# Performance work log

Hardware: AMD Instinct MI355X
Metric: run time of the kernel (lower is better)

Reference implementation:

```python
import jax, jax.numpy as jnp
import numpy as np

E = 1024
H = 16
DH = E // H
FF = 4 * E
EPS = 1e-5


def _layer_norm(x, g, b):
    mu = jnp.mean(x, axis=-1, keepdims=True)
    var = jnp.var(x, axis=-1, keepdims=True)
    return (x - mu) * jax.lax.rsqrt(var + EPS) * g + b


def setup_inputs() -> dict:
    key = jax.random.key(0)
    ks = jax.random.split(key, 12)
    B, S = 2, 2048
    s_e = 1.0 / np.sqrt(E)
    s_f = 1.0 / np.sqrt(FF)
    return {
        "hidden_states": jax.random.normal(ks[0], (B, S, E), jnp.float32),
        "attention_mask": jnp.zeros((B, S), jnp.float32),
        "position_bias": jax.random.normal(ks[1], (H, S, S), jnp.float32) * 0.1,
        "Wq": jax.random.normal(ks[2], (E, E), jnp.float32) * s_e,
        "bq": jnp.zeros((E,), jnp.float32),
        "Wk": jax.random.normal(ks[3], (E, E), jnp.float32) * s_e,
        "bk": jnp.zeros((E,), jnp.float32),
        "Wv": jax.random.normal(ks[4], (E, E), jnp.float32) * s_e,
        "bv": jnp.zeros((E,), jnp.float32),
        "Wo": jax.random.normal(ks[5], (E, E), jnp.float32) * s_e,
        "bo": jnp.zeros((E,), jnp.float32),
        "ln1_g": jnp.ones((E,), jnp.float32),
        "ln1_b": jnp.zeros((E,), jnp.float32),
        "W1": jax.random.normal(ks[6], (E, FF), jnp.float32) * s_e,
        "b1": jnp.zeros((FF,), jnp.float32),
        "W2": jax.random.normal(ks[7], (FF, E), jnp.float32) * s_f,
        "b2": jnp.zeros((E,), jnp.float32),
        "ln2_g": jnp.ones((E,), jnp.float32),
        "ln2_b": jnp.zeros((E,), jnp.float32),
    }


def reference(hidden_states, attention_mask, position_bias, Wq, bq, Wk, bk, Wv, bv,
              Wo, bo, ln1_g, ln1_b, W1, b1, W2, b2, ln2_g, ln2_b):
    B, S, _ = hidden_states.shape
    x = hidden_states
    # QKV projections, split heads: [B, S, H, DH]
    q = (x @ Wq + bq).reshape(B, S, H, DH)
    k = (x @ Wk + bk).reshape(B, S, H, DH)
    v = (x @ Wv + bv).reshape(B, S, H, DH)
    # scores: [B, H, S, S]
    scores = jnp.einsum("bshd,bthd->bhst", q, k) / np.sqrt(DH).astype(np.float32)
    scores = scores + position_bias[None] + attention_mask[:, None, None, :]
    probs = jax.nn.softmax(scores, axis=-1)  # dropout is identity in eval
    ctx = jnp.einsum("bhst,bthd->bshd", probs, v).reshape(B, S, E)
    attn_out = ctx @ Wo + bo
    h = _layer_norm(x + attn_out, ln1_g, ln1_b)
    ffn = jax.nn.gelu(h @ W1 + b1, approximate=False) @ W2 + b2
    return _layer_norm(h + ffn, ln2_g, ln2_b)
```

## Files before the change

### kernel.cpp

```cpp
#include <hip/hip_runtime.h>
#include <stdint.h>

#define EDIM   1024
#define NHEAD  16
#define DHEAD  64
#define FFDIM  4096
#define SEQLEN 2048
#define NBATCH 2
#define MROWS  (NBATCH * SEQLEN)
#define NT     (SEQLEN / 64)

typedef __attribute__((ext_vector_type(8))) short bf16x8;
typedef __attribute__((ext_vector_type(4))) float f32x4;

static __device__ __forceinline__ unsigned short f2bf(float f) {
    union { float f; uint32_t u; } v; v.f = f;
    return (unsigned short)((v.u + 0x7fffu + ((v.u >> 16) & 1u)) >> 16);
}

static __device__ __forceinline__ void gload16(const void* g, void* s) {
    __builtin_amdgcn_global_load_lds(
        (const __attribute__((address_space(1))) unsigned int*)g,
        (__attribute__((address_space(3))) unsigned int*)s,
        16, 0, 0);
}

static __device__ __forceinline__ float gelu_f(float x) {
    float z = 0.7978845608028654f * (x + 0.044715f * x * x * x);
    float e = __expf(-2.0f * fabsf(z));
    float th = (1.0f - e) / (1.0f + e);
    th = (z >= 0.0f) ? th : -th;
    return 0.5f * x * (1.0f + th);
}

__global__ void k_cast_bf16(const float* __restrict__ in, unsigned short* __restrict__ out, int n4) {
    int i = blockIdx.x * blockDim.x + threadIdx.x;
    if (i < n4) {
        float4 v = ((const float4*)in)[i];
        ushort4 o;
        o.x = f2bf(v.x); o.y = f2bf(v.y); o.z = f2bf(v.z); o.w = f2bf(v.w);
        ((ushort4*)out)[i] = o;
    }
}

__global__ void k_transpose_cast(const float* __restrict__ in, unsigned short* __restrict__ out,
                                 int R, int C) {
    __shared__ float tile[32][33];
    int c0 = blockIdx.x * 32, r0 = blockIdx.y * 32;
    int tx = threadIdx.x, ty = threadIdx.y;
    #pragma unroll
    for (int i = 0; i < 32; i += 8)
        tile[ty + i][tx] = in[(size_t)(r0 + ty + i) * C + c0 + tx];
    __syncthreads();
    #pragma unroll
    for (int i = 0; i < 32; i += 8)
        out[(size_t)(c0 + ty + i) * R + r0 + tx] = f2bf(tile[tx][ty + i]);
}

__global__ void k_transpose_cast4(const float* __restrict__ s0, const float* __restrict__ s1,
                                  const float* __restrict__ s2, const float* __restrict__ s3,
                                  unsigned short* __restrict__ d0, unsigned short* __restrict__ d1,
                                  unsigned short* __restrict__ d2, unsigned short* __restrict__ d3) {
    __shared__ float tile[32][33];
    const int z = blockIdx.z;
    const float* in = (z == 0) ? s0 : (z == 1) ? s1 : (z == 2) ? s2 : s3;
    unsigned short* out = (z == 0) ? d0 : (z == 1) ? d1 : (z == 2) ? d2 : d3;
    int c0 = blockIdx.x * 32, r0 = blockIdx.y * 32;
    int tx = threadIdx.x, ty = threadIdx.y;
    #pragma unroll
    for (int i = 0; i < 32; i += 8)
        tile[ty + i][tx] = in[(size_t)(r0 + ty + i) * EDIM + c0 + tx];
    __syncthreads();
    #pragma unroll
    for (int i = 0; i < 32; i += 8)
        out[(size_t)(c0 + ty + i) * EDIM + r0 + tx] = f2bf(tile[tx][ty + i]);
}

__global__ void k_transpose_v(const unsigned short* __restrict__ V, int vstride,
                              unsigned short* __restrict__ Vt) {
    __shared__ unsigned short tile[32][33];
    const int bh = blockIdx.z, b = bh >> 4, h = bh & 15;
    const int s0 = blockIdx.x * 32, d0 = blockIdx.y * 32;
    const int tx = threadIdx.x, ty = threadIdx.y;
    #pragma unroll
    for (int i = 0; i < 32; i += 8)
        tile[ty + i][tx] = V[(size_t)(b * SEQLEN + s0 + ty + i) * vstride + h * DHEAD + d0 + tx];
    __syncthreads();
    #pragma unroll
    for (int i = 0; i < 32; i += 8)
        Vt[((size_t)(b * NHEAD + h) * DHEAD + d0 + ty + i) * SEQLEN + s0 + tx] = tile[tx][ty + i];
}

__global__ void k_concat_bias(const float* __restrict__ bq, const float* __restrict__ bk,
                              const float* __restrict__ bv, float* __restrict__ out) {
    int i = blockIdx.x * 256 + threadIdx.x;
    const float* src = (i < 1024) ? bq : (i < 2048) ? bk : bv;
    out[i] = src[i & 1023];
}

template <int TBM, int TBN, int EPI, int SPLITK>
__global__ __launch_bounds__(256, 3) void k_gemm(
    const unsigned short* __restrict__ A,
    const unsigned short* __restrict__ Bt,
    const float* __restrict__ bias,
    void* __restrict__ Cout, int M, int N, int K)
{
    constexpr int MR = TBM / 32, NR = TBN / 32;
    __shared__ __attribute__((aligned(16))) unsigned short Asm[TBM * 64];
    __shared__ __attribute__((aligned(16))) unsigned short Bsm[TBN * 64];

    const int nbx = gridDim.x;
    const int flat = blockIdx.y * nbx + blockIdx.x;
    const int cpx = (nbx * gridDim.y) >> 3;
    const int swz = (flat & 7) * cpx + (flat >> 3);
    const int bx = swz % nbx, by = swz / nbx;
    const int kz = (SPLITK > 1) ? blockIdx.z : 0;
    const int Ksub = K / SPLITK;

    const int row0 = by * TBM, col0 = bx * TBN;
    const int t = threadIdx.x;
    const int lane = t & 63, w = t >> 6;
    const int wm = w >> 1, wn = w & 1;
    const int l15 = lane & 15, l4 = lane >> 4;
    const int sr = lane >> 3, sc = (lane & 7) * 8;

    f32x4 acc[MR][NR];
    #pragma unroll
    for (int m = 0; m < MR; ++m)
        #pragma unroll
        for (int n = 0; n < NR; ++n) acc[m][n] = (f32x4){0.f, 0.f, 0.f, 0.f};

    for (int k0 = kz * Ksub; k0 < (kz + 1) * Ksub; k0 += 64) {
        #pragma unroll
        for (int i = 0; i < TBM / 32; ++i) {
            const int r = w * (TBM / 4) + i * 8;
            gload16(A + (size_t)(row0 + r + sr) * K + k0 + sc, &Asm[r * 64]);
        }
        #pragma unroll
        for (int i = 0; i < TBN / 32; ++i) {
            const int r = w * (TBN / 4) + i * 8;
            gload16(Bt + (size_t)(col0 + r + sr) * K + k0 + sc, &Bsm[r * 64]);
        }
        __syncthreads();
        #pragma unroll
        for (int kk = 0; kk < 64; kk += 32) {
            bf16x8 af[MR], bf[NR];
            #pragma unroll
            for (int m = 0; m < MR; ++m)
                af[m] = *(const bf16x8*)&Asm[(wm * (TBM / 2) + m * 16 + l15) * 64 + kk + l4 * 8];
            #pragma unroll
            for (int n = 0; n < NR; ++n)
                bf[n] = *(const bf16x8*)&Bsm[(wn * (TBN / 2) + n * 16 + l15) * 64 + kk + l4 * 8];
            #pragma unroll
            for (int m = 0; m < MR; ++m)
                #pragma unroll
                for (int n = 0; n < NR; ++n)
                    acc[m][n] = __builtin_amdgcn_mfma_f32_16x16x32_bf16(af[m], bf[n], acc[m][n], 0, 0, 0);
        }
        __syncthreads();
    }

    #pragma unroll
    for (int m = 0; m < MR; ++m) {
        int rb = row0 + wm * (TBM / 2) + m * 16 + l4 * 4;
        #pragma unroll
        for (int n = 0; n < NR; ++n) {
            int c = col0 + wn * (TBN / 2) + n * 16 + l15;
            float bv = (SPLITK == 1 || kz == 0) ? bias[c] : 0.0f;
            #pragma unroll
            for (int i = 0; i < 4; ++i) {
                float v = acc[m][n][i] + bv;
                if (EPI == 1) v = gelu_f(v);
                if (EPI == 2) {
                    float* outp = (float*)Cout + (size_t)kz * M * N;
                    outp[(size_t)(rb + i) * N + c] = v;
                } else {
                    ((unsigned short*)Cout)[(size_t)(rb + i) * N + c] = f2bf(v);
                }
            }
        }
    }
}

__global__ __launch_bounds__(512, 2) void k_gemm256(
    const unsigned short* __restrict__ A,
    const unsigned short* __restrict__ Bt,
    const float* __restrict__ bias,
    unsigned short* __restrict__ C, int M, int N, int K)
{
    __shared__ __attribute__((aligned(16))) unsigned short Asm[2][2][256 * 32];
    __shared__ __attribute__((aligned(16))) unsigned short Bsm[2][2][256 * 32];

    const int nbx = gridDim.x;
    const int flat = blockIdx.y * nbx + blockIdx.x;
    const int cpx = (nbx * gridDim.y) >> 3;
    const int swz = (flat & 7) * cpx + (flat >> 3);
    const int bx = swz % nbx, by = swz / nbx;
    const int row0 = by * 256, col0 = bx * 256;

    const int t = threadIdx.x;
    const int lane = t & 63, w = t >> 6;
    const int wm = w >> 2, wn = w & 3;
    const int l15 = lane & 15, l4 = lane >> 4;
    const int NTK = K / 64;

    f32x4 acc[8][4];
    #pragma unroll
    for (int m = 0; m < 8; ++m)
        #pragma unroll
        for (int n = 0; n < 4; ++n) acc[m][n] = (f32x4){0.f, 0.f, 0.f, 0.f};

    auto stage = [&](int nb, int h, int T) {
        const int k0 = T * 64 + h * 32;
        #pragma unroll
        for (int j = 0; j < 2; ++j) {
            const int sb = j * 512 + w * 64;
            const int slot = sb + lane;
            const int r = slot >> 2;
            const int cs = (slot & 3) ^ (r & 3);
            gload16(A + (size_t)(row0 + r) * K + k0 + cs * 8, &Asm[nb][h][sb * 8]);
        }
        #pragma unroll
        for (int j = 0; j < 2; ++j) {
            const int sb = j * 512 + w * 64;
            const int slot = sb + lane;
            const int r = slot >> 2;
            const int cs = (slot & 3) ^ (r & 3);
            gload16(Bt + (size_t)(col0 + r) * K + k0 + cs * 8, &Bsm[nb][h][sb * 8]);
        }
    };

    auto compute = [&](int buf, int h) {
        const int ch = (l4 ^ (l15 & 3)) << 3;
        bf16x8 bfr[4];
        #pragma unroll
        for (int n = 0; n < 4; ++n)
            bfr[n] = *(const bf16x8*)&Bsm[buf][h][(wn * 64 + n * 16 + l15) * 32 + ch];
        bf16x8 afr[8];
        #pragma unroll
        for (int m = 0; m < 8; ++m)
            afr[m] = *(const bf16x8*)&Asm[buf][h][(wm * 128 + m * 16 + l15) * 32 + ch];
        __builtin_amdgcn_s_setprio(1);
        #pragma unroll
        for (int m = 0; m < 8; ++m)
            #pragma unroll
            for (int n = 0; n < 4; ++n)
                acc[m][n] = __builtin_amdgcn_mfma_f32_16x16x32_bf16(afr[m], bfr[n], acc[m][n], 0, 0, 0);
        __builtin_amdgcn_s_setprio(0);
    };

    stage(0, 0, 0);
    stage(0, 1, 0);

    for (int T = 0; T < NTK; ++T) {
        const int buf = T & 1, nb = buf ^ 1;
        const int Tn = (T + 1) & (NTK - 1);
        asm volatile("s_waitcnt vmcnt(4)" ::: "memory");
        __builtin_amdgcn_s_barrier();
        stage(nb, 0, Tn);
        compute(buf, 0);
        asm volatile("s_waitcnt vmcnt(4)" ::: "memory");
        __builtin_amdgcn_s_barrier();
        stage(nb, 1, Tn);
        compute(buf, 1);
    }

    #pragma unroll
    for (int m = 0; m < 8; ++m) {
        const int rb = row0 + wm * 128 + m * 16 + l4 * 4;
        #pragma unroll
        for (int n = 0; n < 4; ++n) {
            const int c = col0 + wn * 64 + n * 16 + l15;
            const float bv = bias[c];
            #pragma unroll
            for (int i = 0; i < 4; ++i) {
                float v = gelu_f(acc[m][n][i] + bv);
                C[(size_t)(rb + i) * N + c] = f2bf(v);
            }
        }
    }
}

__global__ __launch_bounds__(512, 3) void k_attn(
    const unsigned short* __restrict__ QKV,
    const unsigned short* __restrict__ Vt,
    const float* __restrict__ pbias,
    const float* __restrict__ mask,
    unsigned short* __restrict__ Ctx)
{
    __shared__ __attribute__((aligned(16))) unsigned short Ksm[2][64 * 64];
    __shared__ __attribute__((aligned(16))) unsigned short Vsm[2][64 * 64];
    __shared__ __attribute__((aligned(16))) unsigned short Psm[8][16 * 32];

    const int flat = blockIdx.x;
    const int swz = (flat & 7) * 64 + (flat >> 3);
    const int h   = swz >> 5;
    const int rem = swz & 31;
    const int b   = rem & 1;
    const int qt  = rem >> 1;

    const int t = threadIdx.x;
    const int lane = t & 63, w = t >> 6;
    const int l15 = lane & 15, l4 = lane >> 4;
    const int qrow = qt * 128 + w * 16;

    const float* pbrow = pbias + ((size_t)h * SEQLEN + qrow + l4 * 4) * SEQLEN;
    const float* mrow  = mask + b * SEQLEN;

    bf16x8 qf0, qf1;
    {
        const unsigned short* qp = QKV + (size_t)(b * SEQLEN + qrow + l15) * (3 * EDIM) + h * DHEAD + l4 * 8;
        bf16x8 r0 = *(const bf16x8*)qp;
        bf16x8 r1 = *(const bf16x8*)(qp + 32);
        #pragma unroll
        for (int e = 0; e < 8; ++e) {
            union { uint32_t u; float f; } c0, c1;
            c0.u = (uint32_t)(unsigned short)r0[e] << 16;
            c1.u = (uint32_t)(unsigned short)r1[e] << 16;
            r0[e] = (short)f2bf(c0.f * 0.125f);
            r1[e] = (short)f2bf(c1.f * 0.125f);
        }
        qf0 = r0; qf1 = r1;
    }

    f32x4 oacc[4];
    #pragma unroll
    for (int nd = 0; nd < 4; ++nd) oacc[nd] = (f32x4){0.f, 0.f, 0.f, 0.f};
    float m_run[4] = {-1e30f, -1e30f, -1e30f, -1e30f};
    float l_run[4] = {0.f, 0.f, 0.f, 0.f};

    const int srow = lane >> 3;
    const int schk = lane & 7;
    const int r7 = l15 & 7;

    auto stage = [&](int buf, int kt) {
        const int kbase = kt * 64;
        #pragma unroll
        for (int j = 0; j < 2; ++j) {
            const int q  = w * 2 + j;
            const int kv = q >> 3;
            const int g  = q & 7;
            const int row = g * 8 + srow;
            const int cg  = (schk ^ (row & 7)) * 8;
            if (kv == 0)
                gload16(QKV + (size_t)(b * SEQLEN + kbase + row) * (3 * EDIM) + EDIM + h * DHEAD + cg,
                        &Ksm[buf][g * 512]);
            else
                gload16(Vt + ((size_t)((b * NHEAD + h) * DHEAD) + row) * SEQLEN + kbase + cg,
                        &Vsm[buf][g * 512]);
        }
    };

    auto compute = [&](int buf, int kt) {
        const int kbase = kt * 64;
        float p[4][4];
        float tmax[4] = {-1e30f, -1e30f, -1e30f, -1e30f};
        #pragma unroll
        for (int n = 0; n < 4; ++n) {
            const int scol = kbase + n * 16 + l15;
            const float mk = mrow[scol];
            f32x4 z;
            #pragma unroll
            for (int i = 0; i < 4; ++i) z[i] = pbrow[(size_t)i * SEQLEN + scol] + mk;
            bf16x8 kb0 = *(const bf16x8*)&Ksm[buf][(n * 16 + l15) * 64 + ((l4 ^ r7) << 3)];
            bf16x8 kb1 = *(const bf16x8*)&Ksm[buf][(n * 16 + l15) * 64 + (((4 + l4) ^ r7) << 3)];
            z = __builtin_amdgcn_mfma_f32_16x16x32_bf16(qf0, kb0, z, 0, 0, 0);
            z = __builtin_amdgcn_mfma_f32_16x16x32_bf16(qf1, kb1, z, 0, 0, 0);
            #pragma unroll
            for (int i = 0; i < 4; ++i) {
                p[n][i] = z[i];
                tmax[i] = fmaxf(tmax[i], z[i]);
            }
        }
        float pmax[4];
        #pragma unroll
        for (int i = 0; i < 4; ++i) pmax[i] = tmax[i];
        #pragma unroll
        for (int off = 1; off < 16; off <<= 1) {
            #pragma unroll
            for (int i = 0; i < 4; ++i) pmax[i] = fmaxf(pmax[i], __shfl_xor(pmax[i], off, 64));
        }
        int need = 0;
        #pragma unroll
        for (int i = 0; i < 4; ++i) need |= (pmax[i] > m_run[i] + 8.0f) ? 1 : 0;
        if (__any(need)) {
            #pragma unroll
            for (int i = 0; i < 4; ++i) {
                float mnew = fmaxf(m_run[i], pmax[i]);
                float alpha = __expf(m_run[i] - mnew);
                m_run[i] = mnew;
                l_run[i] *= alpha;
                #pragma unroll
                for (int nd = 0; nd < 4; ++nd) oacc[nd][i] *= alpha;
            }
        }
        #pragma unroll
        for (int i = 0; i < 4; ++i) {
            float sum = 0.f;
            #pragma unroll
            for (int n = 0; n < 4; ++n) { p[n][i] = __expf(p[n][i] - m_run[i]); sum += p[n][i]; }
            #pragma unroll
            for (int off = 1; off < 16; off <<= 1) sum += __shfl_xor(sum, off, 64);
            l_run[i] += sum;
        }
        #pragma unroll
        for (int hh = 0; hh < 2; ++hh) {
            #pragma unroll
            for (int n = 0; n < 2; ++n)
                #pragma unroll
                for (int i = 0; i < 4; ++i) {
                    const int row = l4 * 4 + i;
                    const int cl = n * 16 + l15;
                    Psm[w][row * 32 + (((cl >> 3) ^ (row & 3)) << 3) + (cl & 7)] =
                        f2bf(p[2 * hh + n][i]);
                }
            bf16x8 pa = *(const bf16x8*)&Psm[w][l15 * 32 + ((l4 ^ (l15 & 3)) << 3)];
            #pragma unroll
            for (int nd = 0; nd < 4; ++nd) {
                bf16x8 vf = *(const bf16x8*)&Vsm[buf][(nd * 16 + l15) * 64 + (((hh * 4 + l4) ^ r7) << 3)];
                oacc[nd] = __builtin_amdgcn_mfma_f32_16x16x32_bf16(pa, vf, oacc[nd], 0, 0, 0);
            }
        }
    };

    stage(0, 0);
    __syncthreads();
    int buf = 0;
    for (int kt = 0; kt < NT; ++kt) {
        stage(buf ^ 1, (kt + 1) & (NT - 1));
        compute(buf, kt);
        __syncthreads();
        buf ^= 1;
    }

    #pragma unroll
    for (int nd = 0; nd < 4; ++nd)
        #pragma unroll
        for (int i = 0; i < 4; ++i) {
            float v = oacc[nd][i] / l_run[i];
            Ctx[(size_t)(b * SEQLEN + qrow + l4 * 4 + i) * EDIM + h * DHEAD + nd * 16 + l15] = f2bf(v);
        }
}

template <int WRITE_BF>
__global__ __launch_bounds__(256) void k_ln(
    const float* __restrict__ X, const float* __restrict__ T, const float* __restrict__ T2,
    const float* __restrict__ gam, const float* __restrict__ bet,
    float* __restrict__ Of, unsigned short* __restrict__ Ob)
{
    const int r = blockIdx.x;
    const int t = threadIdx.x;
    const size_t base = (size_t)r * EDIM + t * 4;
    float4 xv = *(const float4*)(X + base);
    float4 tv = *(const float4*)(T + base);
    float4 t2 = *(const float4*)(T2 + base);
    float4 s = make_float4(xv.x + tv.x + t2.x, xv.y + tv.y + t2.y,
                           xv.z + tv.z + t2.z, xv.w + tv.w + t2.w);
    float sum = s.x + s.y + s.z + s.w;
    float sq  = s.x * s.x + s.y * s.y + s.z * s.z + s.w * s.w;
    #pragma unroll
    for (int off = 1; off < 64; off <<= 1) {
        sum += __shfl_xor(sum, off, 64);
        sq  += __shfl_xor(sq,  off, 64);
    }
    __shared__ float red[8];
    const int lane = t & 63, w = t >> 6;
    if (lane == 0) { red[w] = sum; red[4 + w] = sq; }
    __syncthreads();
    sum = red[0] + red[1] + red[2] + red[3];
    sq  = red[4] + red[5] + red[6] + red[7];
    const float mu = sum * (1.0f / EDIM);
    const float var = sq * (1.0f / EDIM) - mu * mu;
    const float rs = rsqrtf(var + 1e-5f);
    float4 gv = *(const float4*)(gam + t * 4);
    float4 bv = *(const float4*)(bet + t * 4);
    float4 o = make_float4((s.x - mu) * rs * gv.x + bv.x,
                           (s.y - mu) * rs * gv.y + bv.y,
                           (s.z - mu) * rs * gv.z + bv.z,
                           (s.w - mu) * rs * gv.w + bv.w);
    *(float4*)(Of + base) = o;
    if (WRITE_BF) {
        ushort4 ob;
        ob.x = f2bf(o.x); ob.y = f2bf(o.y); ob.z = f2bf(o.z); ob.w = f2bf(o.w);
        *(ushort4*)(Ob + base) = ob;
    }
}

extern "C" void kernel_launch(void* const* d_in, const int* in_sizes, int n_in,
                              void* d_out, int out_size, void* d_ws, size_t ws_size,
                              hipStream_t stream) {
    const float* x    = (const float*)d_in[0];
    const float* mask = (const float*)d_in[1];
    const float* pb   = (const float*)d_in[2];
    const float* Wq = (const float*)d_in[3];  const float* bq = (const float*)d_in[4];
    const float* Wk = (const float*)d_in[5];  const float* bk = (const float*)d_in[6];
    const float* Wv = (const float*)d_in[7];  const float* bv = (const float*)d_in[8];
    const float* Wo = (const float*)d_in[9];  const float* bo = (const float*)d_in[10];
    const float* g1 = (const float*)d_in[11]; const float* be1 = (const float*)d_in[12];
    const float* W1 = (const float*)d_in[13]; const float* b1 = (const float*)d_in[14];
    const float* W2 = (const float*)d_in[15]; const float* b2 = (const float*)d_in[16];
    const float* g2 = (const float*)d_in[17]; const float* be2 = (const float*)d_in[18];
    float* out = (float*)d_out;

    char* ws = (char*)d_ws;
    const size_t MB = 1024 * 1024;
    unsigned short* qkv  = (unsigned short*)(ws + 0);
    unsigned short* gbf  = (unsigned short*)(ws + 0);
    unsigned short* wqt  = (unsigned short*)(ws + 32 * MB);
    unsigned short* wkt  = (unsigned short*)(ws + 34 * MB);
    unsigned short* wvt  = (unsigned short*)(ws + 36 * MB);
    unsigned short* wot  = (unsigned short*)(ws + 38 * MB);
    unsigned short* w1t  = (unsigned short*)(ws + 40 * MB);
    unsigned short* w2t  = (unsigned short*)(ws + 48 * MB);
    float*          bcat = (float*)(ws + 56 * MB);
    unsigned short* ctxb = (unsigned short*)(ws + 56 * MB);
    unsigned short* xb   = (unsigned short*)(ws + 64 * MB);
    unsigned short* vt   = (unsigned short*)(ws + 64 * MB);
    float*          pt0  = (float*)(ws + 72 * MB);
    float*          pt1  = (float*)(ws + 88 * MB);
    float*          hf   = (float*)(ws + 104 * MB);
    unsigned short* hb   = (unsigned short*)(ws + 120 * MB);

    const dim3 b256(256);
    const dim3 tb(32, 8);

    k_cast_bf16<<<dim3(MROWS * EDIM / 4 / 256), b256, 0, stream>>>(x, xb, MROWS * EDIM / 4);
    k_transpose_cast4<<<dim3(EDIM / 32, EDIM / 32, 4), tb, 0, stream>>>(
        Wq, Wk, Wv, Wo, wqt, wkt, wvt, wot);
    k_transpose_cast<<<dim3(FFDIM / 32, EDIM / 32), tb, 0, stream>>>(W1, w1t, EDIM, FFDIM);
    k_transpose_cast<<<dim3(EDIM / 32, FFDIM / 32), tb, 0, stream>>>(W2, w2t, FFDIM, EDIM);
    k_concat_bias<<<dim3(12), b256, 0, stream>>>(bq, bk, bv, bcat);

    k_gemm<128, 128, 0, 1><<<dim3(3 * EDIM / 128, MROWS / 128), b256, 0, stream>>>(
        xb, wqt, bcat, qkv, MROWS, 3 * EDIM, EDIM);
    k_transpose_v<<<dim3(SEQLEN / 32, DHEAD / 32, NBATCH * NHEAD), tb, 0, stream>>>(
        qkv + 2 * EDIM, 3 * EDIM, vt);

    k_attn<<<dim3(512), dim3(512), 0, stream>>>(qkv, vt, pb, mask, ctxb);

    k_gemm<128, 128, 2, 2><<<dim3(EDIM / 128, MROWS / 128, 2), b256, 0, stream>>>(
        ctxb, wot, bo, pt0, MROWS, EDIM, EDIM);
    k_ln<1><<<dim3(MROWS), b256, 0, stream>>>(x, pt0, pt1, g1, be1, hf, hb);
    k_gemm256<<<dim3(FFDIM / 256, MROWS / 256), dim3(512), 0, stream>>>(
        hb, w1t, b1, gbf, MROWS, FFDIM, EDIM);
    k_gemm<128, 128, 2, 2><<<dim3(EDIM / 128, MROWS / 128, 2), b256, 0, stream>>>(
        gbf, w2t, b2, pt0, MROWS, EDIM, FFDIM);
    k_ln<0><<<dim3(MROWS), b256, 0, stream>>>(hf, pt0, pt1, g2, be2, out, nullptr);
    (void)in_sizes; (void)n_in; (void)out_size; (void)ws_size;
}
```

Before: 344.1 us.

## Double-buffer 128x128 GEMM with XOR-swizzled LDS and async prefetch

Replaces the single-buffered 128x128 GEMM with a version that double-buffers LDS in two K-halves. It issues global-to-LDS loads for the next tile while computing the current one, with explicit vmcnt waits and barriers. LDS rows are XOR-swizzled to reduce bank conflicts, and MFMA issue gets higher priority. Doubling LDS use lowers occupancy (launch bounds drop from 3 to 2 blocks per SM), and the wrapped prefetch on the last iteration does a redundant load.

```diff
diff --git a/kernel.cpp b/kernel.cpp
--- a/kernel.cpp
+++ b/kernel.cpp
@@ -98,79 +98,103 @@
     out[i] = src[i & 1023];
 }
 
-template <int TBM, int TBN, int EPI, int SPLITK>
-__global__ __launch_bounds__(256, 3) void k_gemm(
+template <int EPI, int SPLITK>
+__global__ __launch_bounds__(256, 2) void k_gemm_cv(
     const unsigned short* __restrict__ A,
     const unsigned short* __restrict__ Bt,
     const float* __restrict__ bias,
     void* __restrict__ Cout, int M, int N, int K)
 {
-    constexpr int MR = TBM / 32, NR = TBN / 32;
-    __shared__ __attribute__((aligned(16))) unsigned short Asm[TBM * 64];
-    __shared__ __attribute__((aligned(16))) unsigned short Bsm[TBN * 64];
+    __shared__ __attribute__((aligned(16))) unsigned short Asm[2][2][128 * 32];
+    __shared__ __attribute__((aligned(16))) unsigned short Bsm[2][2][128 * 32];
 
     const int nbx = gridDim.x;
     const int flat = blockIdx.y * nbx + blockIdx.x;
     const int cpx = (nbx * gridDim.y) >> 3;
     const int swz = (flat & 7) * cpx + (flat >> 3);
     const int bx = swz % nbx, by = swz / nbx;
+    const int row0 = by * 128, col0 = bx * 128;
     const int kz = (SPLITK > 1) ? blockIdx.z : 0;
     const int Ksub = K / SPLITK;
-
-    const int row0 = by * TBM, col0 = bx * TBN;
+    const int kbase0 = kz * Ksub;
+    const int NTK = Ksub / 64;
+
     const int t = threadIdx.x;
     const int lane = t & 63, w = t >> 6;
     const int wm = w >> 1, wn = w & 1;
     const int l15 = lane & 15, l4 = lane >> 4;
-    const int sr = lane >> 3, sc = (lane & 7) * 8;
-
-    f32x4 acc[MR][NR];
-    #pragma unroll
-    for (int m = 0; m < MR; ++m)
-        #pragma unroll
-        for (int n = 0; n < NR; ++n) acc[m][n] = (f32x4){0.f, 0.f, 0.f, 0.f};
-
-    for (int k0 = kz * Ksub; k0 < (kz + 1) * Ksub; k0 += 64) {
-        #pragma unroll
-        for (int i = 0; i < TBM / 32; ++i) {
-            const int r = w * (TBM / 4) + i * 8;
-            gload16(A + (size_t)(row0 + r + sr) * K + k0 + sc, &Asm[r * 64]);
-        }
-        #pragma unroll
-        for (int i = 0; i < TBN / 32; ++i) {
-            const int r = w * (TBN / 4) + i * 8;
-            gload16(Bt + (size_t)(col0 + r + sr) * K + k0 + sc, &Bsm[r * 64]);
-        }
-        __syncthreads();
-        #pragma unroll
-        for (int kk = 0; kk < 64; kk += 32) {
-            bf16x8 af[MR], bf[NR];
-            #pragma unroll
-            for (int m = 0; m < MR; ++m)
-                af[m] = *(const bf16x8*)&Asm[(wm * (TBM / 2) + m * 16 + l15) * 64 + kk + l4 * 8];
-            #pragma unroll
-            for (int n = 0; n < NR; ++n)
-                bf[n] = *(const bf16x8*)&Bsm[(wn * (TBN / 2) + n * 16 + l15) * 64 + kk + l4 * 8];
-            #pragma unroll
-            for (int m = 0; m < MR; ++m)
-                #pragma unroll
-                for (int n = 0; n < NR; ++n)
-                    acc[m][n] = __builtin_amdgcn_mfma_f32_16x16x32_bf16(af[m], bf[n], acc[m][n], 0, 0, 0);
-        }
-        __syncthreads();
-    }
-
-    #pragma unroll
-    for (int m = 0; m < MR; ++m) {
-        int rb = row0 + wm * (TBM / 2) + m * 16 + l4 * 4;
-        #pragma unroll
-        for (int n = 0; n < NR; ++n) {
-            int c = col0 + wn * (TBN / 2) + n * 16 + l15;
-            float bv = (SPLITK == 1 || kz == 0) ? bias[c] : 0.0f;
+
+    f32x4 acc[4][4];
+    #pragma unroll
+    for (int m = 0; m < 4; ++m)
+        #pragma unroll
+        for (int n = 0; n < 4; ++n) acc[m][n] = (f32x4){0.f, 0.f, 0.f, 0.f};
+
+    auto stage = [&](int nb, int h, int T) {
+        const int k0 = kbase0 + T * 64 + h * 32;
+        #pragma unroll
+        for (int j = 0; j < 2; ++j) {
+            const int sb = j * 256 + w * 64;
+            const int slot = sb + lane;
+            const int r = slot >> 2;
+            const int cs = (slot & 3) ^ (r & 3);
+            gload16(A + (size_t)(row0 + r) * K + k0 + cs * 8, &Asm[nb][h][sb * 8]);
+        }
+        #pragma unroll
+        for (int j = 0; j < 2; ++j) {
+            const int sb = j * 256 + w * 64;
+            const int slot = sb + lane;
+            const int r = slot >> 2;
+            const int cs = (slot & 3) ^ (r & 3);
+            gload16(Bt + (size_t)(col0 + r) * K + k0 + cs * 8, &Bsm[nb][h][sb * 8]);
+        }
+    };
+
+    auto compute = [&](int buf, int h) {
+        const int ch = (l4 ^ (l15 & 3)) << 3;
+        bf16x8 bfr[4];
+        #pragma unroll
+        for (int n = 0; n < 4; ++n)
+            bfr[n] = *(const bf16x8*)&Bsm[buf][h][(wn * 64 + n * 16 + l15) * 32 + ch];
+        bf16x8 afr[4];
+        #pragma unroll
+        for (int m = 0; m < 4; ++m)
+            afr[m] = *(const bf16x8*)&Asm[buf][h][(wm * 64 + m * 16 + l15) * 32 + ch];
+        __builtin_amdgcn_s_setprio(1);
+        #pragma unroll
+        for (int m = 0; m < 4; ++m)
+            #pragma unroll
+            for (int n = 0; n < 4; ++n)
+                acc[m][n] = __builtin_amdgcn_mfma_f32_16x16x32_bf16(afr[m], bfr[n], acc[m][n], 0, 0, 0);
+        __builtin_amdgcn_s_setprio(0);
+    };
+
+    stage(0, 0, 0);
+    stage(0, 1, 0);
+
+    for (int T = 0; T < NTK; ++T) {
+        const int buf = T & 1, nb = buf ^ 1;
+        const int Tn = (T + 1) & (NTK - 1);
+        asm volatile("s_waitcnt vmcnt(4)" ::: "memory");
+        __builtin_amdgcn_s_barrier();
+        stage(nb, 0, Tn);
+        compute(buf, 0);
+        asm volatile("s_waitcnt vmcnt(4)" ::: "memory");
+        __builtin_amdgcn_s_barrier();
+        stage(nb, 1, Tn);
+        compute(buf, 1);
+    }
+
+    #pragma unroll
+    for (int m = 0; m < 4; ++m) {
+        const int rb = row0 + wm * 64 + m * 16 + l4 * 4;
+        #pragma unroll
+        for (int n = 0; n < 4; ++n) {
+            const int c = col0 + wn * 64 + n * 16 + l15;
+            const float bv = (SPLITK == 1 || kz == 0) ? bias[c] : 0.0f;
             #pragma unroll
             for (int i = 0; i < 4; ++i) {
                 float v = acc[m][n][i] + bv;
-                if (EPI == 1) v = gelu_f(v);
                 if (EPI == 2) {
                     float* outp = (float*)Cout + (size_t)kz * M * N;
                     outp[(size_t)(rb + i) * N + c] = v;
@@ -531,19 +555,19 @@
     k_transpose_cast<<<dim3(EDIM / 32, FFDIM / 32), tb, 0, stream>>>(W2, w2t, FFDIM, EDIM);
     k_concat_bias<<<dim3(12), b256, 0, stream>>>(bq, bk, bv, bcat);
 
-    k_gemm<128, 128, 0, 1><<<dim3(3 * EDIM / 128, MROWS / 128), b256, 0, stream>>>(
+    k_gemm_cv<0, 1><<<dim3(3 * EDIM / 128, MROWS / 128), b256, 0, stream>>>(
         xb, wqt, bcat, qkv, MROWS, 3 * EDIM, EDIM);
     k_transpose_v<<<dim3(SEQLEN / 32, DHEAD / 32, NBATCH * NHEAD), tb, 0, stream>>>(
         qkv + 2 * EDIM, 3 * EDIM, vt);
 
     k_attn<<<dim3(512), dim3(512), 0, stream>>>(qkv, vt, pb, mask, ctxb);
 
-    k_gemm<128, 128, 2, 2><<<dim3(EDIM / 128, MROWS / 128, 2), b256, 0, stream>>>(
+    k_gemm_cv<2, 2><<<dim3(EDIM / 128, MROWS / 128, 2), b256, 0, stream>>>(
         ctxb, wot, bo, pt0, MROWS, EDIM, EDIM);
     k_ln<1><<<dim3(MROWS), b256, 0, stream>>>(x, pt0, pt1, g1, be1, hf, hb);
     k_gemm256<<<dim3(FFDIM / 256, MROWS / 256), dim3(512), 0, stream>>>(
         hb, w1t, b1, gbf, MROWS, FFDIM, EDIM);
-    k_gemm<128, 128, 2, 2><<<dim3(EDIM / 128, MROWS / 128, 2), b256, 0, stream>>>(
+    k_gemm_cv<2, 2><<<dim3(EDIM / 128, MROWS / 128, 2), b256, 0, stream>>>(
         gbf, w2t, b2, pt0, MROWS, EDIM, FFDIM);
     k_ln<0><<<dim3(MROWS), b256, 0, stream>>>(hf, pt0, pt1, g2, be2, out, nullptr);
     (void)in_sizes; (void)n_in; (void)out_size; (void)ws_size;
```

Result: slower. 361.5 us (+5.0%).
